# Kernel optimization log

Measured on AMD Instinct MI355X. Metric: run time of the kernel, lower is better.

Reference implementation:

```python
import jax, jax.numpy as jnp
import numpy as np
import math

FACTOR = 5  # Informer 'factor' hyperparameter


def setup_inputs() -> dict:
    key = jax.random.key(0)
    B, L, H, D = 2, 2048, 16, 128
    k1, k2, k3, k4 = jax.random.split(key, 4)
    queries = jax.random.normal(k1, (B, L, H, D), jnp.float32)
    keys = jax.random.normal(k2, (B, L, H, D), jnp.float32)
    values = jax.random.normal(k3, (B, L, H, D), jnp.float32)
    sample_k = max(1, min(FACTOR * math.ceil(math.log(L)), L))  # u in the paper
    index_sample = jax.random.randint(k4, (L, sample_k), 0, L, dtype=jnp.int32)
    return {"queries": queries, "keys": keys, "values": values,
            "index_sample": index_sample}


def reference(queries, keys, values, index_sample):
    # queries/keys/values: [B, L, H, D] -> [B, H, L, D]
    Q = jnp.swapaxes(queries, 1, 2)
    K = jnp.swapaxes(keys, 1, 2)
    V = jnp.swapaxes(values, 1, 2)
    B, H, L_Q, D = Q.shape
    L_K = K.shape[2]
    # U_part = factor*ceil(ln L_K), clipped to L_K then to L_Q (n_top in _prob_QK)
    n_top = max(1, min(FACTOR * math.ceil(math.log(L_K)), L_K, L_Q))

    # --- _prob_QK: sampled scores ---
    # K_sample: [B, H, L_Q, sample_k, D] (same materialization as torch K_expand gather)
    K_sample = K[:, :, index_sample, :]
    Q_K_sample = jnp.einsum('bhqd,bhqsd->bhqs', Q, K_sample)
    # sparsity measure M: max - mean(over full L_K, per original torch code)
    M = Q_K_sample.max(axis=-1) - Q_K_sample.sum(axis=-1) / L_K  # [B,H,L_Q]
    _, M_top = jax.lax.top_k(M, n_top)  # [B,H,n_top]

    # gather top queries and compute their full attention rows
    Q_reduce = jnp.take_along_axis(Q, M_top[..., None], axis=2)  # [B,H,u,D]
    scores = jnp.einsum('bhud,bhkd->bhuk', Q_reduce, K)  # [B,H,u,L_K]
    scale = 1.0 / math.sqrt(D)
    scores = scores * scale

    # --- initial context (mask_flag=False): mean of V over keys ---
    context = jnp.broadcast_to(V.mean(axis=2, keepdims=True), (B, H, L_Q, D))

    # --- update context at top-query positions ---
    attn = jax.nn.softmax(scores, axis=-1)
    upd = jnp.einsum('bhuk,bhkd->bhud', attn, V)  # [B,H,u,D]
    bi = jnp.arange(B)[:, None, None]
    hi = jnp.arange(H)[None, :, None]
    context = context.at[bi, hi, M_top].set(upd)

    return jnp.swapaxes(context, 1, 2)  # [B, L_Q, H, D]
```

## Files before the change

kernel.cpp:

```cpp
#include <hip/hip_runtime.h>
#include <math.h>

#define B_    2
#define L_    2048
#define H_    16
#define D_    128
#define S_    40
#define NTOP_ 40
#define NCH_  8
#define CHK_  256
#define VCH_  32
#define CAND_ 512

#define SCALE_ 0.08838834764831843f

typedef _Float16 half2_t __attribute__((ext_vector_type(2)));

__device__ __forceinline__ half2_t as_h2(unsigned int u) {
    union { unsigned int u; half2_t h; } x; x.u = u; return x.h;
}
__device__ __forceinline__ unsigned int h2pack(float a, float b) {
    union { half2_t h; unsigned int u; } x;
    x.h[0] = (_Float16)a; x.h[1] = (_Float16)b; return x.u;
}
#if __has_builtin(__builtin_amdgcn_fdot2)
__device__ __forceinline__ float FDOT2(half2_t a, half2_t b, float c) {
    return __builtin_amdgcn_fdot2(a, b, c, false);
}
#else
__device__ __forceinline__ float FDOT2(half2_t a, half2_t b, float c) {
    return c + (float)a[0] * (float)b[0] + (float)a[1] * (float)b[1];
}
#endif

__device__ __forceinline__ unsigned int encf(float f) {
    unsigned int u = __float_as_uint(f);
    return (u & 0x80000000u) ? ~u : (u | 0x80000000u);
}
__device__ __forceinline__ float decf(unsigned int e) {
    unsigned int u = (e & 0x80000000u) ? (e ^ 0x80000000u) : ~e;
    return __uint_as_float(u);
}

__global__ __launch_bounds__(256) void kpack(const float* __restrict__ K,
                                             unsigned int* __restrict__ Kf) {
    const int bid = blockIdx.x, t = threadIdx.x;
    const int bh = bid >> 3, kc = bid & 7;
    const int h = bh & 15, b = bh >> 4;
    const float4* K4 = (const float4*)K;
    uint2* out2 = (uint2*)Kf;
    for (int j = 0; j < 32; ++j) {
        const int g = j * 256 + t;
        const int row = g >> 5, c = g & 31;
        const float4 v = K4[((size_t)(b * L_ + kc * 256 + row) * H_ + h) * 32 + c];
        out2[(size_t)(bh * L_ + kc * 256 + row) * 32 + c] =
            make_uint2(h2pack(v.x, v.y), h2pack(v.z, v.w));
    }
}

__global__ __launch_bounds__(256) void k1_sample_f16(const float* __restrict__ Q,
                                                     const uint4* __restrict__ KF,
                                                     const float* __restrict__ V,
                                                     const int* __restrict__ idx,
                                                     float* __restrict__ M,
                                                     float* __restrict__ vpart) {
    const int bid = blockIdx.x;
    const int t   = threadIdx.x;

    if (bid < 1024) {
        __shared__ float red[256];
        const int vbid = bid;
        const int bh  = vbid >> 5;
        const int lc  = vbid & (VCH_ - 1);
        const int h   = bh & 15, b = bh >> 4;
        const int d   = t & (D_ - 1);
        const int sub = t >> 7;
        float acc = 0.0f;
        const int l0 = lc * (L_ / VCH_);
        for (int l = l0 + sub; l < l0 + L_ / VCH_; l += 2)
            acc += V[((size_t)(b * L_ + l) * H_ + h) * D_ + d];
        red[t] = acc;
        __syncthreads();
        if (t < D_) vpart[(size_t)vbid * D_ + t] = red[t] + red[t + 128];
        return;
    }

    const int sb   = bid - 1024;
    const int xcd  = sb & 7;
    const int li   = sb >> 3;
    const int bh   = (xcd << 2) + (li >> 9);
    const int rb   = li & 511;
    const int wave = t >> 6, lane = t & 63;
    const int q    = rb * 4 + wave;
    const int h    = bh & 15, b = bh >> 4;
    const int g    = lane >> 3, sub = lane & 7;

    const float4* Q4 = (const float4*)Q;
    const size_t rowQ = ((size_t)(b * L_ + q) * H_ + h) * 32;
    const int* ip = idx + q * S_;
    int kidx[5];
    #pragma unroll
    for (int s = 0; s < 5; ++s) kidx[s] = ip[s * 8 + g];

    const float4 qa0 = Q4[rowQ + 2 * sub];
    const float4 qa1 = Q4[rowQ + 2 * sub + 1];
    const float4 qb0 = Q4[rowQ + 16 + 2 * sub];
    const float4 qb1 = Q4[rowQ + 16 + 2 * sub + 1];

    uint4 kv[5][2];
    #pragma unroll
    for (int s = 0; s < 5; ++s) {
        const uint4* kr = KF + ((size_t)bh * L_ + kidx[s]) * 16;
        kv[s][0] = kr[sub];
        kv[s][1] = kr[8 + sub];
    }
    __builtin_amdgcn_sched_barrier(0);

    half2_t qh[8];
    qh[0][0] = (_Float16)qa0.x; qh[0][1] = (_Float16)qa0.y;
    qh[1][0] = (_Float16)qa0.z; qh[1][1] = (_Float16)qa0.w;
    qh[2][0] = (_Float16)qa1.x; qh[2][1] = (_Float16)qa1.y;
    qh[3][0] = (_Float16)qa1.z; qh[3][1] = (_Float16)qa1.w;
    qh[4][0] = (_Float16)qb0.x; qh[4][1] = (_Float16)qb0.y;
    qh[5][0] = (_Float16)qb0.z; qh[5][1] = (_Float16)qb0.w;
    qh[6][0] = (_Float16)qb1.x; qh[6][1] = (_Float16)qb1.y;
    qh[7][0] = (_Float16)qb1.z; qh[7][1] = (_Float16)qb1.w;

    float smax = -INFINITY, ssum = 0.0f;
    #pragma unroll
    for (int s = 0; s < 5; ++s) {
        float p = 0.f;
        p = FDOT2(qh[0], as_h2(kv[s][0].x), p);
        p = FDOT2(qh[1], as_h2(kv[s][0].y), p);
        p = FDOT2(qh[2], as_h2(kv[s][0].z), p);
        p = FDOT2(qh[3], as_h2(kv[s][0].w), p);
        p = FDOT2(qh[4], as_h2(kv[s][1].x), p);
        p = FDOT2(qh[5], as_h2(kv[s][1].y), p);
        p = FDOT2(qh[6], as_h2(kv[s][1].z), p);
        p = FDOT2(qh[7], as_h2(kv[s][1].w), p);
        p += __shfl_xor(p, 1);
        p += __shfl_xor(p, 2);
        p += __shfl_xor(p, 4);
        smax = fmaxf(smax, p);
        ssum += p;
    }
    #pragma unroll
    for (int o = 8; o < 64; o <<= 1) {
        smax = fmaxf(smax, __shfl_xor(smax, o));
        ssum += __shfl_xor(ssum, o);
    }
    if (lane == 0) M[(size_t)bh * L_ + q] = smax - ssum * (1.0f / L_);
}

__global__ __launch_bounds__(256) void k1_sample_f32(const float* __restrict__ Q,
                                                     const float* __restrict__ K,
                                                     const float* __restrict__ V,
                                                     const int* __restrict__ idx,
                                                     float* __restrict__ M,
                                                     float* __restrict__ vpart) {
    const int bid = blockIdx.x;
    const int t   = threadIdx.x;
    if (bid < 1024) {
        __shared__ float red[256];
        const int vbid = bid;
        const int bh  = vbid >> 5;
        const int lc  = vbid & (VCH_ - 1);
        const int h   = bh & 15, b = bh >> 4;
        const int d   = t & (D_ - 1);
        const int sub = t >> 7;
        float acc = 0.0f;
        const int l0 = lc * (L_ / VCH_);
        for (int l = l0 + sub; l < l0 + L_ / VCH_; l += 2)
            acc += V[((size_t)(b * L_ + l) * H_ + h) * D_ + d];
        red[t] = acc;
        __syncthreads();
        if (t < D_) vpart[(size_t)vbid * D_ + t] = red[t] + red[t + 128];
        return;
    }
    const int sb   = bid - 1024;
    const int xcd  = sb & 7;
    const int li   = sb >> 3;
    const int bh   = (xcd << 2) + (li >> 9);
    const int rb   = li & 511;
    const int wave = t >> 6, lane = t & 63;
    const int q    = rb * 4 + wave;
    const int h    = bh & 15, b = bh >> 4;
    const int g    = lane >> 3, sub = lane & 7;

    const float4* Q4 = (const float4*)Q;
    const float4* K4 = (const float4*)K;
    const size_t rowQ = ((size_t)(b * L_ + q) * H_ + h) * 32;
    const size_t kbase = ((size_t)b * L_ * H_ + h) * 32 + sub;
    const int* ip = idx + q * S_;
    int kidx[5];
    #pragma unroll
    for (int s = 0; s < 5; ++s) kidx[s] = ip[s * 8 + g];
    const float4 qv0 = Q4[rowQ + 0 + sub];
    const float4 qv1 = Q4[rowQ + 8 + sub];
    const float4 qv2 = Q4[rowQ + 16 + sub];
    const float4 qv3 = Q4[rowQ + 24 + sub];
    float4 kv[5][4];
    #pragma unroll
    for (int s = 0; s < 5; ++s) {
        const float4* kb = K4 + kbase + (size_t)kidx[s] * (H_ * 32);
        kv[s][0] = kb[0]; kv[s][1] = kb[8]; kv[s][2] = kb[16]; kv[s][3] = kb[24];
    }
    __builtin_amdgcn_sched_barrier(0);
    float smax = -INFINITY, ssum = 0.0f;
    #pragma unroll
    for (int s = 0; s < 5; ++s) {
        float p = qv0.x * kv[s][0].x + qv0.y * kv[s][0].y + qv0.z * kv[s][0].z + qv0.w * kv[s][0].w
                + qv1.x * kv[s][1].x + qv1.y * kv[s][1].y + qv1.z * kv[s][1].z + qv1.w * kv[s][1].w
                + qv2.x * kv[s][2].x + qv2.y * kv[s][2].y + qv2.z * kv[s][2].z + qv2.w * kv[s][2].w
                + qv3.x * kv[s][3].x + qv3.y * kv[s][3].y + qv3.z * kv[s][3].z + qv3.w * kv[s][3].w;
        p += __shfl_xor(p, 1);
        p += __shfl_xor(p, 2);
        p += __shfl_xor(p, 4);
        smax = fmaxf(smax, p);
        ssum += p;
    }
    #pragma unroll
    for (int o = 8; o < 64; o <<= 1) {
        smax = fmaxf(smax, __shfl_xor(smax, o));
        ssum += __shfl_xor(ssum, o);
    }
    if (lane == 0) M[(size_t)bh * L_ + q] = smax - ssum * (1.0f / L_);
}

__global__ __launch_bounds__(1024) void k2_rank_refine_fill(const float* __restrict__ Mws,
                                                            const float* __restrict__ Q,
                                                            const float* __restrict__ K,
                                                            const int* __restrict__ idx,
                                                            const float* __restrict__ vpart,
                                                            int* __restrict__ topk,
                                                            float* __restrict__ out,
                                                            float delta) {
    const int bid = blockIdx.x, t = threadIdx.x;
    if (bid < 32) {
        __shared__ unsigned int ue[L_];
        __shared__ int hist[256], sscan[256];
        __shared__ int sh_chosen, sh_need, sh_nc;
        __shared__ int clist[CAND_];
        __shared__ float cMx[CAND_];
        __shared__ unsigned int cmaxe[CAND_];
        __shared__ float csum[CAND_];
        const int bh = bid, h = bh & 15, b = bh >> 4;
        const float* Mrow = Mws + (size_t)bh * L_;
        for (int i = t; i < L_; i += 1024) ue[i] = encf(Mrow[i]);
        if (t == 0) sh_nc = 0;
        __syncthreads();

        unsigned int prefix = 0; int need = NTOP_;
        for (int l = 3; l >= 0; --l) {
            if (t < 256) hist[t] = 0;
            __syncthreads();
            for (int i = t; i < L_; i += 1024) {
                const unsigned int u = ue[i];
                const bool match = (l == 3) || ((u >> (8 * (l + 1))) == prefix);
                if (match) atomicAdd(&hist[(u >> (8 * l)) & 255], 1);
            }
            __syncthreads();
            if (t < 256) sscan[t] = hist[t];
            __syncthreads();
            for (int off = 1; off < 256; off <<= 1) {
                int v = 0;
                if (t < 256 && t + off < 256) v = sscan[t + off];
                __syncthreads();
                if (t < 256) sscan[t] += v;
                __syncthreads();
            }
            if (t < 256) {
                const int above = sscan[t] - hist[t];
                if (above < need && need <= above + hist[t]) { sh_chosen = t; sh_need = need - above; }
            }
            __syncthreads();
            prefix = (prefix << 8) | (unsigned int)sh_chosen;
            need = sh_need;
            __syncthreads();
        }
        const unsigned int ethr = encf(decf(prefix) - delta);
        for (int i = t; i < L_; i += 1024) {
            if (ue[i] >= ethr) {
                const int p = atomicAdd(&sh_nc, 1);
                if (p < CAND_) clist[p] = i;
            }
        }
        __syncthreads();
        const int nc = min(sh_nc, CAND_);
        for (int i = t; i < CAND_; i += 1024) { cmaxe[i] = 0x007FFFFFu; csum[i] = 0.f; }
        __syncthreads();

        const float4* Q4 = (const float4*)Q;
        const float4* K4 = (const float4*)K;
        const int grp = t >> 3, sub = t & 7;
        for (int task = grp; task < nc * S_; task += 128) {
            const int ci = task / S_;
            const int s  = task - ci * S_;
            const int qq = clist[ci];
            const int ki = idx[qq * S_ + s];
            const float4* Kr = K4 + ((size_t)(b * L_ + ki) * H_ + h) * 32;
            const float4* Qr = Q4 + ((size_t)(b * L_ + qq) * H_ + h) * 32;
            float p = 0.f;
            #pragma unroll
            for (int qt2 = 0; qt2 < 4; ++qt2) {
                const float4 kv = Kr[qt2 * 8 + sub];
                const float4 qv = Qr[qt2 * 8 + sub];
                p += qv.x * kv.x + qv.y * kv.y + qv.z * kv.z + qv.w * kv.w;
            }
            p += __shfl_xor(p, 1);
            p += __shfl_xor(p, 2);
            p += __shfl_xor(p, 4);
            if (sub == 0) {
                atomicMax(&cmaxe[ci], encf(p));
                atomicAdd(&csum[ci], p);
            }
        }
        __syncthreads();
        if (t < nc) cMx[t] = decf(cmaxe[t]) - csum[t] * (1.0f / L_);
        __syncthreads();
        if (t < nc) {
            const float mi = cMx[t]; const int qi = clist[t];
            int rk = 0;
            for (int j = 0; j < nc; ++j) {
                const float mj = cMx[j];
                rk += (mj > mi) || (mj == mi && clist[j] < qi);
            }
            if (rk < NTOP_) topk[bh * NTOP_ + rk] = qi;
        }
    } else {
        __shared__ float red[1024];
        __shared__ float vmf[128];
        const int fb = bid - 32;
        const int bh = fb >> 4, sl = fb & 15;
        const int h = bh & 15, b = bh >> 4;
        const int d = t & 127, grp = t >> 7;
        float s = 0.f;
        #pragma unroll
        for (int c = grp * 4; c < grp * 4 + 4; ++c)
            s += vpart[(size_t)(bh * VCH_ + c) * D_ + d];
        red[t] = s;
        __syncthreads();
        if (t < 512) red[t] += red[t + 512];
        __syncthreads();
        if (t < 256) red[t] += red[t + 256];
        __syncthreads();
        if (t < 128) vmf[t] = (red[t] + red[t + 128]) * (1.0f / L_);
        __syncthreads();
        const float4 vm4 = *(const float4*)&vmf[(t & 31) * 4];
        float4* out4 = (float4*)out;
        const int q0 = sl * 128;
        #pragma unroll
        for (int k = 0; k < 4; ++k) {
            const int j = k * 1024 + t;
            const int r = j >> 5, c = j & 31;
            out4[((size_t)(b * L_ + q0 + r) * H_ + h) * 32 + c] = vm4;
        }
    }
}

__global__ __launch_bounds__(256) void k_scorepv(const float* __restrict__ Q,
                                                 const float* __restrict__ K,
                                                 const float* __restrict__ V,
                                                 const int* __restrict__ topk,
                                                 float* __restrict__ pmax,
                                                 float* __restrict__ psum,
                                                 float* __restrict__ pout) {
    __shared__ float Qs[20 * 132];
    __shared__ float S[20 * 260];
    __shared__ float mrow[20];
    __shared__ int   tq[20];
    const int bid = blockIdx.x;
    const int xcd = bid & 7;
    const int loc = bid >> 3;
    const int bh  = (xcd << 2) + (loc >> 4);
    const int sub16 = loc & 15;
    const int kc  = sub16 >> 1;
    const int uh  = sub16 & 1;
    const int h   = bh & 15, b = bh >> 4;
    const int t   = threadIdx.x;

    if (t < 20) tq[t] = topk[bh * NTOP_ + uh * 20 + t];
    __syncthreads();

    {
        const float4* Q4 = (const float4*)Q;
        #pragma unroll
        for (int it = 0; it < 3; ++it) {
            const int i = it * 256 + t;
            if (i < 640) {
                const int u = i >> 5, dc = i & 31;
                *(float4*)&Qs[u * 132 + dc * 4] =
                    Q4[((size_t)(b * L_ + tq[u]) * H_ + h) * 32 + dc];
            }
        }
    }
    __syncthreads();

    {
        const int kq4 = t >> 2, ug = t & 3;
        float acc[4][5];
        #pragma unroll
        for (int j = 0; j < 4; ++j)
            #pragma unroll
            for (int uu = 0; uu < 5; ++uu) acc[j][uu] = 0.f;
        const float4* Kb = (const float4*)K +
            ((size_t)(b * L_ + kc * CHK_ + kq4 * 4) * H_ + h) * 32;
        for (int dc = 0; dc < 32; ++dc) {
            float4 qv[5];
            #pragma unroll
            for (int uu = 0; uu < 5; ++uu)
                qv[uu] = *(const float4*)&Qs[(ug * 5 + uu) * 132 + dc * 4];
            #pragma unroll
            for (int j = 0; j < 4; ++j) {
                const float4 kv = Kb[(size_t)j * (H_ * 32) + dc];
                #pragma unroll
                for (int uu = 0; uu < 5; ++uu)
                    acc[j][uu] += qv[uu].x * kv.x + qv[uu].y * kv.y
                                + qv[uu].z * kv.z + qv[uu].w * kv.w;
            }
        }
        #pragma unroll
        for (int j = 0; j < 4; ++j)
            #pragma unroll
            for (int uu = 0; uu < 5; ++uu)
                S[(ug * 5 + uu) * 260 + kq4 * 4 + j] = acc[j][uu] * SCALE_;
    }
    __syncthreads();

    {
        const int w = t >> 6, lane = t & 63;
        #pragma unroll
        for (int uu = 0; uu < 5; ++uu) {
            const int u = w * 5 + uu;
            const float* Sr = S + u * 260;
            float v = fmaxf(fmaxf(Sr[lane], Sr[lane + 64]),
                            fmaxf(Sr[lane + 128], Sr[lane + 192]));
            #pragma unroll
            for (int o = 1; o < 64; o <<= 1) v = fmaxf(v, __shfl_xor(v, o, 64));
            if (lane == 0) mrow[u] = v;
        }
    }
    __syncthreads();

    #pragma unroll
    for (int u = 0; u < 20; ++u) S[u * 260 + t] = __expf(S[u * 260 + t] - mrow[u]);
    __syncthreads();

    {
        const int w = t >> 6, lane = t & 63;
        #pragma unroll
        for (int uu = 0; uu < 5; ++uu) {
            const int u = w * 5 + uu;
            const float* Sr = S + u * 260;
            float v = Sr[lane] + Sr[lane + 64] + Sr[lane + 128] + Sr[lane + 192];
            #pragma unroll
            for (int o = 1; o < 64; o <<= 1) v += __shfl_xor(v, o, 64);
            if (lane == 0) {
                psum[(bh * NCH_ + kc) * NTOP_ + uh * 20 + u] = v;
                pmax[(bh * NCH_ + kc) * NTOP_ + uh * 20 + u] = mrow[u];
            }
        }
    }

    {
        const int g = t >> 6, d2 = t & 63;
        const int u0 = g * 5;
        float accA[5], accB[5];
        #pragma unroll
        for (int uu = 0; uu < 5; ++uu) { accA[uu] = 0.f; accB[uu] = 0.f; }
        const float2* Vb = (const float2*)(V + ((size_t)(b * L_ + kc * CHK_) * H_ + h) * D_) + d2;
        for (int kq = 0; kq < CHK_ / 4; ++kq) {
            float2 v0 = Vb[(size_t)(kq * 4 + 0) * (H_ * D_ / 2)];
            float2 v1 = Vb[(size_t)(kq * 4 + 1) * (H_ * D_ / 2)];
            float2 v2 = Vb[(size_t)(kq * 4 + 2) * (H_ * D_ / 2)];
            float2 v3 = Vb[(size_t)(kq * 4 + 3) * (H_ * D_ / 2)];
            #pragma unroll
            for (int uu = 0; uu < 5; ++uu) {
                const float4 p = *(const float4*)&S[(u0 + uu) * 260 + kq * 4];
                accA[uu] += p.x * v0.x + p.y * v1.x + p.z * v2.x + p.w * v3.x;
                accB[uu] += p.x * v0.y + p.y * v1.y + p.z * v2.y + p.w * v3.y;
            }
        }
        float* pb = pout + (((size_t)(bh * NCH_ + kc)) * NTOP_ + uh * 20 + u0) * D_ + d2 * 2;
        #pragma unroll
        for (int uu = 0; uu < 5; ++uu)
            *(float2*)&pb[(size_t)uu * D_] = make_float2(accA[uu], accB[uu]);
    }
}

__global__ __launch_bounds__(128) void k_comb(const float* __restrict__ pmax,
                                              const float* __restrict__ psum,
                                              const float* __restrict__ pout,
                                              const int* __restrict__ topk,
                                              float* __restrict__ out) {
    const int bid = blockIdx.x;
    const int bh  = bid / NTOP_;
    const int u   = bid - bh * NTOP_;
    const int h   = bh & 15, b = bh >> 4;
    const int t   = threadIdx.x;

    float pm[NCH_];
    float M = -INFINITY;
    #pragma unroll
    for (int c = 0; c < NCH_; ++c) {
        pm[c] = pmax[(bh * NCH_ + c) * NTOP_ + u];
        M = fmaxf(M, pm[c]);
    }
    float ssum = 0.0f, o = 0.0f;
    #pragma unroll
    for (int c = 0; c < NCH_; ++c) {
        const float w = __expf(pm[c] - M);
        ssum += psum[(bh * NCH_ + c) * NTOP_ + u] * w;
        o += pout[((size_t)(bh * NCH_ + c) * NTOP_ + u) * D_ + t] * w;
    }
    const int qi = topk[bh * NTOP_ + u];
    out[((size_t)(b * L_ + qi) * H_ + h) * D_ + t] = o / ssum;
}

extern "C" void kernel_launch(void* const* d_in, const int* in_sizes, int n_in,
                              void* d_out, int out_size, void* d_ws, size_t ws_size,
                              hipStream_t stream) {
    const float* Q  = (const float*)d_in[0];
    const float* K  = (const float*)d_in[1];
    const float* V  = (const float*)d_in[2];
    const int* idx  = (const int*)d_in[3];
    float* out      = (float*)d_out;

    char* ws = (char*)d_ws;
    size_t off = 0;
    float* Mws   = (float*)(ws + off); off += (size_t)65536 * 4;
    float* vpart = (float*)(ws + off); off += (size_t)1024 * 128 * 4;
    int*   topk  = (int*)(ws + off);   off += 1280 * 4;
    float* pmax  = (float*)(ws + off); off += (size_t)256 * 40 * 4;
    float* psum  = (float*)(ws + off); off += (size_t)256 * 40 * 4;
    float* pout  = (float*)(ws + off); off += (size_t)256 * 40 * 128 * 4;
    unsigned int* Kf = (unsigned int*)(ws + off);
    const size_t kf_bytes = (size_t)32 * L_ * D_ * 2;
    const bool use_f16 = (ws_size >= off + kf_bytes);

    if (use_f16) {
        hipLaunchKernelGGL(kpack, dim3(256), dim3(256), 0, stream, K, Kf);
        hipLaunchKernelGGL(k1_sample_f16, dim3(1024 + 16384), dim3(256), 0, stream,
                           Q, (const uint4*)Kf, V, idx, Mws, vpart);
    } else {
        hipLaunchKernelGGL(k1_sample_f32, dim3(1024 + 16384), dim3(256), 0, stream,
                           Q, K, V, idx, Mws, vpart);
    }
    hipLaunchKernelGGL(k2_rank_refine_fill, dim3(32 + 512), dim3(1024), 0, stream,
                       Mws, Q, K, idx, vpart, topk, out, use_f16 ? 0.5f : 0.01f);
    hipLaunchKernelGGL(k_scorepv, dim3(512), dim3(256), 0, stream,
                       Q, K, V, topk, pmax, psum, pout);
    hipLaunchKernelGGL(k_comb, dim3(1280), dim3(128), 0, stream,
                       pmax, psum, pout, topk, out);
}
```

Before: 127.4 us.

## Rebalance kernel fusion: pair V-mean with K pack, fill with score-PV

```diff
diff --git a/kernel.cpp b/kernel.cpp
--- a/kernel.cpp
+++ b/kernel.cpp
@@ -42,34 +42,27 @@
     return __uint_as_float(u);
 }
 
-__global__ __launch_bounds__(256) void kpack(const float* __restrict__ K,
-                                             unsigned int* __restrict__ Kf) {
+__global__ __launch_bounds__(256) void kA_pack_vpart(const float* __restrict__ K,
+                                                     const float* __restrict__ V,
+                                                     unsigned int* __restrict__ Kf,
+                                                     float* __restrict__ vpart,
+                                                     int npack) {
     const int bid = blockIdx.x, t = threadIdx.x;
-    const int bh = bid >> 3, kc = bid & 7;
-    const int h = bh & 15, b = bh >> 4;
-    const float4* K4 = (const float4*)K;
-    uint2* out2 = (uint2*)Kf;
-    for (int j = 0; j < 32; ++j) {
-        const int g = j * 256 + t;
-        const int row = g >> 5, c = g & 31;
-        const float4 v = K4[((size_t)(b * L_ + kc * 256 + row) * H_ + h) * 32 + c];
-        out2[(size_t)(bh * L_ + kc * 256 + row) * 32 + c] =
-            make_uint2(h2pack(v.x, v.y), h2pack(v.z, v.w));
-    }
-}
-
-__global__ __launch_bounds__(256) void k1_sample_f16(const float* __restrict__ Q,
-                                                     const uint4* __restrict__ KF,
-                                                     const float* __restrict__ V,
-                                                     const int* __restrict__ idx,
-                                                     float* __restrict__ M,
-                                                     float* __restrict__ vpart) {
-    const int bid = blockIdx.x;
-    const int t   = threadIdx.x;
-
-    if (bid < 1024) {
+    if (bid < npack) {
+        const int bh = bid >> 3, kc = bid & 7;
+        const int h = bh & 15, b = bh >> 4;
+        const float4* K4 = (const float4*)K;
+        uint2* out2 = (uint2*)Kf;
+        for (int j = 0; j < 32; ++j) {
+            const int g = j * 256 + t;
+            const int row = g >> 5, c = g & 31;
+            const float4 v = K4[((size_t)(b * L_ + kc * 256 + row) * H_ + h) * 32 + c];
+            out2[(size_t)(bh * L_ + kc * 256 + row) * 32 + c] =
+                make_uint2(h2pack(v.x, v.y), h2pack(v.z, v.w));
+        }
+    } else {
         __shared__ float red[256];
-        const int vbid = bid;
+        const int vbid = bid - npack;
         const int bh  = vbid >> 5;
         const int lc  = vbid & (VCH_ - 1);
         const int h   = bh & 15, b = bh >> 4;
@@ -82,14 +75,19 @@
         red[t] = acc;
         __syncthreads();
         if (t < D_) vpart[(size_t)vbid * D_ + t] = red[t] + red[t + 128];
-        return;
-    }
-
-    const int sb   = bid - 1024;
+    }
+}
+
+__global__ __launch_bounds__(256) void k1_sample_f16(const float* __restrict__ Q,
+                                                     const uint4* __restrict__ KF,
+                                                     const int* __restrict__ idx,
+                                                     float* __restrict__ M) {
+    const int sb   = blockIdx.x;
     const int xcd  = sb & 7;
     const int li   = sb >> 3;
     const int bh   = (xcd << 2) + (li >> 9);
     const int rb   = li & 511;
+    const int t    = threadIdx.x;
     const int wave = t >> 6, lane = t & 63;
     const int q    = rb * 4 + wave;
     const int h    = bh & 15, b = bh >> 4;
@@ -154,34 +152,14 @@
 
 __global__ __launch_bounds__(256) void k1_sample_f32(const float* __restrict__ Q,
                                                      const float* __restrict__ K,
-                                                     const float* __restrict__ V,
                                                      const int* __restrict__ idx,
-                                                     float* __restrict__ M,
-                                                     float* __restrict__ vpart) {
-    const int bid = blockIdx.x;
-    const int t   = threadIdx.x;
-    if (bid < 1024) {
-        __shared__ float red[256];
-        const int vbid = bid;
-        const int bh  = vbid >> 5;
-        const int lc  = vbid & (VCH_ - 1);
-        const int h   = bh & 15, b = bh >> 4;
-        const int d   = t & (D_ - 1);
-        const int sub = t >> 7;
-        float acc = 0.0f;
-        const int l0 = lc * (L_ / VCH_);
-        for (int l = l0 + sub; l < l0 + L_ / VCH_; l += 2)
-            acc += V[((size_t)(b * L_ + l) * H_ + h) * D_ + d];
-        red[t] = acc;
-        __syncthreads();
-        if (t < D_) vpart[(size_t)vbid * D_ + t] = red[t] + red[t + 128];
-        return;
-    }
-    const int sb   = bid - 1024;
+                                                     float* __restrict__ M) {
+    const int sb   = blockIdx.x;
     const int xcd  = sb & 7;
     const int li   = sb >> 3;
     const int bh   = (xcd << 2) + (li >> 9);
     const int rb   = li & 511;
+    const int t    = threadIdx.x;
     const int wave = t >> 6, lane = t & 63;
     const int q    = rb * 4 + wave;
     const int h    = bh & 15, b = bh >> 4;
@@ -227,157 +205,153 @@
     if (lane == 0) M[(size_t)bh * L_ + q] = smax - ssum * (1.0f / L_);
 }
 
-__global__ __launch_bounds__(1024) void k2_rank_refine_fill(const float* __restrict__ Mws,
-                                                            const float* __restrict__ Q,
-                                                            const float* __restrict__ K,
-                                                            const int* __restrict__ idx,
-                                                            const float* __restrict__ vpart,
-                                                            int* __restrict__ topk,
-                                                            float* __restrict__ out,
-                                                            float delta) {
+__global__ __launch_bounds__(1024) void k2_rank_refine(const float* __restrict__ Mws,
+                                                       const float* __restrict__ Q,
+                                                       const float* __restrict__ K,
+                                                       const int* __restrict__ idx,
+                                                       int* __restrict__ topk,
+                                                       float delta) {
+    __shared__ unsigned int ue[L_];
+    __shared__ int hist[256], sscan[256];
+    __shared__ int sh_chosen, sh_need, sh_nc;
+    __shared__ int clist[CAND_];
+    __shared__ float cMx[CAND_];
+    __shared__ unsigned int cmaxe[CAND_];
+    __shared__ float csum[CAND_];
     const int bid = blockIdx.x, t = threadIdx.x;
-    if (bid < 32) {
-        __shared__ unsigned int ue[L_];
-        __shared__ int hist[256], sscan[256];
-        __shared__ int sh_chosen, sh_need, sh_nc;
-        __shared__ int clist[CAND_];
-        __shared__ float cMx[CAND_];
-        __shared__ unsigned int cmaxe[CAND_];
-        __shared__ float csum[CAND_];
-        const int bh = bid, h = bh & 15, b = bh >> 4;
-        const float* Mrow = Mws + (size_t)bh * L_;
-        for (int i = t; i < L_; i += 1024) ue[i] = encf(Mrow[i]);
-        if (t == 0) sh_nc = 0;
-        __syncthreads();
-
-        unsigned int prefix = 0; int need = NTOP_;
-        for (int l = 3; l >= 0; --l) {
-            if (t < 256) hist[t] = 0;
+    const int bh = bid, h = bh & 15, b = bh >> 4;
+    const float* Mrow = Mws + (size_t)bh * L_;
+    for (int i = t; i < L_; i += 1024) ue[i] = encf(Mrow[i]);
+    if (t == 0) sh_nc = 0;
+    __syncthreads();
+
+    unsigned int prefix = 0; int need = NTOP_;
+    for (int l = 3; l >= 0; --l) {
+        if (t < 256) hist[t] = 0;
+        __syncthreads();
+        for (int i = t; i < L_; i += 1024) {
+            const unsigned int u = ue[i];
+            const bool match = (l == 3) || ((u >> (8 * (l + 1))) == prefix);
+            if (match) atomicAdd(&hist[(u >> (8 * l)) & 255], 1);
+        }
+        __syncthreads();
+        if (t < 256) sscan[t] = hist[t];
+        __syncthreads();
+        for (int off = 1; off < 256; off <<= 1) {
+            int v = 0;
+            if (t < 256 && t + off < 256) v = sscan[t + off];
             __syncthreads();
-            for (int i = t; i < L_; i += 1024) {
-                const unsigned int u = ue[i];
-                const bool match = (l == 3) || ((u >> (8 * (l + 1))) == prefix);
-                if (match) atomicAdd(&hist[(u >> (8 * l)) & 255], 1);
-            }
+            if (t < 256) sscan[t] += v;
             __syncthreads();
-            if (t < 256) sscan[t] = hist[t];
-            __syncthreads();
-            for (int off = 1; off < 256; off <<= 1) {
-                int v = 0;
-                if (t < 256 && t + off < 256) v = sscan[t + off];
-                __syncthreads();
-                if (t < 256) sscan[t] += v;
-                __syncthreads();
-            }
-            if (t < 256) {
-                const int above = sscan[t] - hist[t];
-                if (above < need && need <= above + hist[t]) { sh_chosen = t; sh_need = need - above; }
-            }
-            __syncthreads();
-            prefix = (prefix << 8) | (unsigned int)sh_chosen;
-            need = sh_need;
-            __syncthreads();
-        }
-        const unsigned int ethr = encf(decf(prefix) - delta);
-        for (int i = t; i < L_; i += 1024) {
-            if (ue[i] >= ethr) {
-                const int p = atomicAdd(&sh_nc, 1);
-                if (p < CAND_) clist[p] = i;
-            }
-        }
-        __syncthreads();
-        const int nc = min(sh_nc, CAND_);
-        for (int i = t; i < CAND_; i += 1024) { cmaxe[i] = 0x007FFFFFu; csum[i] = 0.f; }
-        __syncthreads();
-
-        const float4* Q4 = (const float4*)Q;
-        const float4* K4 = (const float4*)K;
-        const int grp = t >> 3, sub = t & 7;
-        for (int task = grp; task < nc * S_; task += 128) {
-            const int ci = task / S_;
-            const int s  = task - ci * S_;
-            const int qq = clist[ci];
-            const int ki = idx[qq * S_ + s];
-            const float4* Kr = K4 + ((size_t)(b * L_ + ki) * H_ + h) * 32;
-            const float4* Qr = Q4 + ((size_t)(b * L_ + qq) * H_ + h) * 32;
-            float p = 0.f;
-            #pragma unroll
-            for (int qt2 = 0; qt2 < 4; ++qt2) {
-                const float4 kv = Kr[qt2 * 8 + sub];
-                const float4 qv = Qr[qt2 * 8 + sub];
-                p += qv.x * kv.x + qv.y * kv.y + qv.z * kv.z + qv.w * kv.w;
-            }
-            p += __shfl_xor(p, 1);
-            p += __shfl_xor(p, 2);
-            p += __shfl_xor(p, 4);
-            if (sub == 0) {
-                atomicMax(&cmaxe[ci], encf(p));
-                atomicAdd(&csum[ci], p);
-            }
-        }
-        __syncthreads();
-        if (t < nc) cMx[t] = decf(cmaxe[t]) - csum[t] * (1.0f / L_);
-        __syncthreads();
-        if (t < nc) {
-            const float mi = cMx[t]; const int qi = clist[t];
-            int rk = 0;
-            for (int j = 0; j < nc; ++j) {
-                const float mj = cMx[j];
-                rk += (mj > mi) || (mj == mi && clist[j] < qi);
-            }
-            if (rk < NTOP_) topk[bh * NTOP_ + rk] = qi;
-        }
-    } else {
-        __shared__ float red[1024];
-        __shared__ float vmf[128];
-        const int fb = bid - 32;
-        const int bh = fb >> 4, sl = fb & 15;
-        const int h = bh & 15, b = bh >> 4;
-        const int d = t & 127, grp = t >> 7;
-        float s = 0.f;
-        #pragma unroll
-        for (int c = grp * 4; c < grp * 4 + 4; ++c)
-            s += vpart[(size_t)(bh * VCH_ + c) * D_ + d];
-        red[t] = s;
-        __syncthreads();
-        if (t < 512) red[t] += red[t + 512];
-        __syncthreads();
-        if (t < 256) red[t] += red[t + 256];
-        __syncthreads();
-        if (t < 128) vmf[t] = (red[t] + red[t + 128]) * (1.0f / L_);
-        __syncthreads();
-        const float4 vm4 = *(const float4*)&vmf[(t & 31) * 4];
-        float4* out4 = (float4*)out;
-        const int q0 = sl * 128;
-        #pragma unroll
-        for (int k = 0; k < 4; ++k) {
-            const int j = k * 1024 + t;
-            const int r = j >> 5, c = j & 31;
-            out4[((size_t)(b * L_ + q0 + r) * H_ + h) * 32 + c] = vm4;
-        }
-    }
-}
-
-__global__ __launch_bounds__(256) void k_scorepv(const float* __restrict__ Q,
-                                                 const float* __restrict__ K,
-                                                 const float* __restrict__ V,
-                                                 const int* __restrict__ topk,
-                                                 float* __restrict__ pmax,
-                                                 float* __restrict__ psum,
-                                                 float* __restrict__ pout) {
+        }
+        if (t < 256) {
+            const int above = sscan[t] - hist[t];
+            if (above < need && need <= above + hist[t]) { sh_chosen = t; sh_need = need - above; }
+        }
+        __syncthreads();
+        prefix = (prefix << 8) | (unsigned int)sh_chosen;
+        need = sh_need;
+        __syncthreads();
+    }
+    const unsigned int ethr = encf(decf(prefix) - delta);
+    for (int i = t; i < L_; i += 1024) {
+        if (ue[i] >= ethr) {
+            const int p = atomicAdd(&sh_nc, 1);
+            if (p < CAND_) clist[p] = i;
+        }
+    }
+    __syncthreads();
+    const int nc = min(sh_nc, CAND_);
+    for (int i = t; i < CAND_; i += 1024) { cmaxe[i] = 0x007FFFFFu; csum[i] = 0.f; }
+    __syncthreads();
+
+    const float4* Q4 = (const float4*)Q;
+    const float4* K4 = (const float4*)K;
+    const int grp = t >> 3, sub = t & 7;
+    for (int task = grp; task < nc * S_; task += 128) {
+        const int ci = task / S_;
+        const int s  = task - ci * S_;
+        const int qq = clist[ci];
+        const int ki = idx[qq * S_ + s];
+        const float4* Kr = K4 + ((size_t)(b * L_ + ki) * H_ + h) * 32;
+        const float4* Qr = Q4 + ((size_t)(b * L_ + qq) * H_ + h) * 32;
+        float p = 0.f;
+        #pragma unroll
+        for (int qt2 = 0; qt2 < 4; ++qt2) {
+            const float4 kv = Kr[qt2 * 8 + sub];
+            const float4 qv = Qr[qt2 * 8 + sub];
+            p += qv.x * kv.x + qv.y * kv.y + qv.z * kv.z + qv.w * kv.w;
+        }
+        p += __shfl_xor(p, 1);
+        p += __shfl_xor(p, 2);
+        p += __shfl_xor(p, 4);
+        if (sub == 0) {
+            atomicMax(&cmaxe[ci], encf(p));
+            atomicAdd(&csum[ci], p);
+        }
+    }
+    __syncthreads();
+    if (t < nc) cMx[t] = decf(cmaxe[t]) - csum[t] * (1.0f / L_);
+    __syncthreads();
+    if (t < nc) {
+        const float mi = cMx[t]; const int qi = clist[t];
+        int rk = 0;
+        for (int j = 0; j < nc; ++j) {
+            const float mj = cMx[j];
+            rk += (mj > mi) || (mj == mi && clist[j] < qi);
+        }
+        if (rk < NTOP_) topk[bh * NTOP_ + rk] = qi;
+    }
+}
+
+__global__ __launch_bounds__(256) void k3_scorepv_fill(const float* __restrict__ Q,
+                                                       const float* __restrict__ K,
+                                                       const float* __restrict__ V,
+                                                       const int* __restrict__ topk,
+                                                       const float* __restrict__ vpart,
+                                                       float* __restrict__ pmax,
+                                                       float* __restrict__ psum,
+                                                       float* __restrict__ pout,
+                                                       float* __restrict__ out) {
     __shared__ float Qs[20 * 132];
     __shared__ float S[20 * 260];
     __shared__ float mrow[20];
     __shared__ int   tq[20];
-    const int bid = blockIdx.x;
-    const int xcd = bid & 7;
-    const int loc = bid >> 3;
+    const int bid0 = blockIdx.x;
+    const int t   = threadIdx.x;
+
+    if (bid0 >= 512) {
+        const int fb = bid0 - 512;
+        const int bh = fb >> 4, sl = fb & 15;
+        const int h = bh & 15, b = bh >> 4;
+        const int d = t & 127, half = t >> 7;
+        float s = 0.f;
+        #pragma unroll
+        for (int c = half * 16; c < half * 16 + 16; ++c)
+            s += vpart[(size_t)(bh * VCH_ + c) * D_ + d];
+        S[t] = s;
+        __syncthreads();
+        if (t < D_) S[t] = (S[t] + S[t + 128]) * (1.0f / L_);
+        __syncthreads();
+        const float4 vm4 = *(const float4*)&S[(t & 31) * 4];
+        float4* out4 = (float4*)out;
+        const int q0 = sl * 128;
+        #pragma unroll
+        for (int k = 0; k < 16; ++k) {
+            const int j = k * 256 + t;
+            const int r = j >> 5, c = j & 31;
+            out4[((size_t)(b * L_ + q0 + r) * H_ + h) * 32 + c] = vm4;
+        }
+        return;
+    }
+
+    const int xcd = bid0 & 7;
+    const int loc = bid0 >> 3;
     const int bh  = (xcd << 2) + (loc >> 4);
     const int sub16 = loc & 15;
     const int kc  = sub16 >> 1;
     const int uh  = sub16 & 1;
     const int h   = bh & 15, b = bh >> 4;
-    const int t   = threadIdx.x;
 
     if (t < 20) tq[t] = topk[bh * NTOP_ + uh * 20 + t];
     __syncthreads();
@@ -539,17 +513,20 @@
     const bool use_f16 = (ws_size >= off + kf_bytes);
 
     if (use_f16) {
-        hipLaunchKernelGGL(kpack, dim3(256), dim3(256), 0, stream, K, Kf);
-        hipLaunchKernelGGL(k1_sample_f16, dim3(1024 + 16384), dim3(256), 0, stream,
-                           Q, (const uint4*)Kf, V, idx, Mws, vpart);
+        hipLaunchKernelGGL(kA_pack_vpart, dim3(256 + 1024), dim3(256), 0, stream,
+                           K, V, Kf, vpart, 256);
+        hipLaunchKernelGGL(k1_sample_f16, dim3(16384), dim3(256), 0, stream,
+                           Q, (const uint4*)Kf, idx, Mws);
     } else {
-        hipLaunchKernelGGL(k1_sample_f32, dim3(1024 + 16384), dim3(256), 0, stream,
-                           Q, K, V, idx, Mws, vpart);
-    }
-    hipLaunchKernelGGL(k2_rank_refine_fill, dim3(32 + 512), dim3(1024), 0, stream,
-                       Mws, Q, K, idx, vpart, topk, out, use_f16 ? 0.5f : 0.01f);
-    hipLaunchKernelGGL(k_scorepv, dim3(512), dim3(256), 0, stream,
-                       Q, K, V, topk, pmax, psum, pout);
+        hipLaunchKernelGGL(kA_pack_vpart, dim3(1024), dim3(256), 0, stream,
+                           K, V, Kf, vpart, 0);
+        hipLaunchKernelGGL(k1_sample_f32, dim3(16384), dim3(256), 0, stream,
+                           Q, K, idx, Mws);
+    }
+    hipLaunchKernelGGL(k2_rank_refine, dim3(32), dim3(1024), 0, stream,
+                       Mws, Q, K, idx, topk, use_f16 ? 0.5f : 0.01f);
+    hipLaunchKernelGGL(k3_scorepv_fill, dim3(1024), dim3(256), 0, stream,
+                       Q, K, V, topk, vpart, pmax, psum, pout, out);
     hipLaunchKernelGGL(k_comb, dim3(1280), dim3(128), 0, stream,
                        pmax, psum, pout, topk, out);
 }
```

Result: slower. 134.6 us (+5.7%).
